# Optimization experiments

Measured on AMD Instinct MI355X. Metric: run time of the kernel, lower is better.

## Reference

```python
import jax, jax.numpy as jnp
import numpy as np

REG_MAX = 16
NC = 80
TOPK = 10
ALPHA = 1.0
BETA = 6.0
BOX_W, CLS_W, DFL_W = 7.5, 0.5, 1.5
IMG = 1280.0


def _ciou(b1, b2, eps=1e-7):
    # b1, b2: [..., 4] xyxy, broadcastable
    b1x1, b1y1, b1x2, b1y2 = b1[..., 0], b1[..., 1], b1[..., 2], b1[..., 3]
    b2x1, b2y1, b2x2, b2y2 = b2[..., 0], b2[..., 1], b2[..., 2], b2[..., 3]
    w1, h1 = b1x2 - b1x1, b1y2 - b1y1
    w2, h2 = b2x2 - b2x1, b2y2 - b2y1
    inter = (jnp.maximum(jnp.minimum(b1x2, b2x2) - jnp.maximum(b1x1, b2x1), 0.0) *
             jnp.maximum(jnp.minimum(b1y2, b2y2) - jnp.maximum(b1y1, b2y1), 0.0))
    union = w1 * h1 + w2 * h2 - inter + eps
    iou = inter / union
    cw = jnp.maximum(b1x2, b2x2) - jnp.minimum(b1x1, b2x1)
    ch = jnp.maximum(b1y2, b2y2) - jnp.minimum(b1y1, b2y1)
    c2 = cw * cw + ch * ch + eps
    rho2 = ((b2x1 + b2x2 - b1x1 - b1x2) ** 2 + (b2y1 + b2y2 - b1y1 - b1y2) ** 2) / 4.0
    v = (4.0 / np.pi ** 2) * (jnp.arctan(w2 / (h2 + eps)) - jnp.arctan(w1 / (h1 + eps))) ** 2
    alpha = jax.lax.stop_gradient(v / (v - iou + (1.0 + eps)))
    return iou - (rho2 / c2 + v * alpha)


def _loss(p0, p1, p2, gt_boxes, gt_labels, strides):
    preds = [p0, p1, p2]
    B = p0.shape[0]
    aps, sts, pds, pcs = [], [], [], []
    for i, p in enumerate(preds):
        H, W = p.shape[2], p.shape[3]
        gy, gx = jnp.meshgrid(jnp.arange(H, dtype=p.dtype) + 0.5,
                              jnp.arange(W, dtype=p.dtype) + 0.5, indexing='ij')
        aps.append(jnp.stack([gx.ravel(), gy.ravel()], -1))          # [HW,2] feat units
        sts.append(jnp.ones((H * W, 1), p.dtype) * strides[i])       # [HW,1]
        pds.append(p[:, :4 * REG_MAX].reshape(B, 4, REG_MAX, H * W).transpose(0, 3, 1, 2))
        pcs.append(p[:, 4 * REG_MAX:].transpose(0, 2, 3, 1).reshape(B, H * W, NC))
    ap = jnp.concatenate(aps)                 # [N,2]
    st = jnp.concatenate(sts)                 # [N,1]
    pred_dist = jnp.concatenate(pds, axis=1)  # [B,N,4,R]
    pred_cls = jnp.concatenate(pcs, axis=1)   # [B,N,NC]
    proj = jnp.arange(REG_MAX, dtype=p0.dtype)
    M = gt_boxes.shape[1]
    N = ap.shape[0]

    def one_image(pd, pc, gb, gl):
        # decode boxes (image units)
        dist = jnp.einsum('nkr,r->nk', jax.nn.softmax(pd, -1), proj)        # [N,4]
        pred_boxes = jnp.concatenate([(ap - dist[:, :2]) * st,
                                      (ap + dist[:, 2:]) * st], -1)          # [N,4]
        # ---- TaskAlignedAssigner (no grad) ----
        sg = jax.lax.stop_gradient
        pb, ps, gbs = sg(pred_boxes), sg(jax.nn.sigmoid(pc)), sg(gb)
        ap_img = ap * st                                                     # [N,2]
        in_gt = ((ap_img[:, None, 0] >= gbs[None, :, 0]) & (ap_img[:, None, 0] <= gbs[None, :, 2]) &
                 (ap_img[:, None, 1] >= gbs[None, :, 1]) & (ap_img[:, None, 1] <= gbs[None, :, 3]))
        ious = jnp.maximum(_ciou(pb[:, None, :], gbs[None, :, :]), 0.0)      # [N,M]
        align = (ps[:, gl] ** ALPHA) * (ious ** BETA) * in_gt
        align = align / (align.max(0, keepdims=True) + 1e-9)
        align = align * (ious > 0.1)
        # topk anchors per GT; anchor takes the GT with max masked score
        #  sequential loop with strict '>' updates)
        vals, idx = jax.lax.top_k(align.T, TOPK)                             # [M,TOPK]
        masked = jnp.zeros((M, N), align.dtype).at[
            jnp.arange(M)[:, None], idx].set(jnp.where(vals > 0, vals, 0.0))
        col = masked.T                                                       # [N,M]
        best_gt = jnp.argmax(col, 1)
        best_score = col.max(1)
        fg = (best_score > 0).astype(pd.dtype)                               # [N]
        num_fg = jnp.maximum(fg.sum(), 1.0)
        labels = gl[best_gt]
        boxes = gbs[best_gt]
        # ---- box (CIoU) loss over fg ----
        box_loss = ((1.0 - _ciou(pred_boxes, boxes)) * fg).sum() / num_fg
        # ---- DFL loss over fg ----
        t = jnp.concatenate([ap - boxes[:, :2] / st, boxes[:, 2:] / st - ap], -1)
        t = jnp.clip(t, 0.0, REG_MAX - 1 - 0.01)   # box2dist clamp
        t = jnp.clip(t, 0.0, REG_MAX - 1e-4)       # DFLLoss clamp
        left = jnp.floor(t).astype(jnp.int32)
        right = jnp.minimum(left + 1, REG_MAX - 1)
        wl = right.astype(t.dtype) - t
        wr = t - left.astype(t.dtype)
        logp = jax.nn.log_softmax(pd, -1)                                    # [N,4,R]
        ce_l = -jnp.take_along_axis(logp, left[..., None], -1)[..., 0]
        ce_r = -jnp.take_along_axis(logp, right[..., None], -1)[..., 0]
        dfl_loss = ((ce_l * wl + ce_r * wr) * fg[:, None]).sum() / (num_fg * 4.0)
        # ---- cls BCE-with-logits over all anchors ----
        cls_t = jax.nn.one_hot(labels, NC, dtype=pc.dtype) * (best_score * fg)[:, None]
        cls_loss = (jnp.logaddexp(0.0, pc) - pc * cls_t).sum(1).mean()
        has_fg = (fg.sum() > 0).astype(pd.dtype)
        return box_loss * has_fg, cls_loss * has_fg, dfl_loss * has_fg

    bl, cl, dl = jax.vmap(one_image)(pred_dist, pred_cls, gt_boxes, gt_labels)
    return BOX_W * bl.sum() + CLS_W * cl.sum() + DFL_W * dl.sum()


def setup_inputs() -> dict:
    key = jax.random.key(0)
    ks = jax.random.split(key, 6)
    p0 = jax.random.normal(ks[0], (8, 144, 160, 160), jnp.float32)
    p1 = jax.random.normal(ks[1], (8, 144, 80, 80), jnp.float32)
    p2 = jax.random.normal(ks[2], (8, 144, 40, 40), jnp.float32)
    cxcy = jax.random.uniform(ks[3], (8, 32, 2), minval=64.0, maxval=IMG - 64.0)
    wh = jax.random.uniform(ks[4], (8, 32, 2), minval=16.0, maxval=256.0)
    gt_boxes = jnp.clip(jnp.concatenate([cxcy - wh / 2, cxcy + wh / 2], -1), 0.0, IMG)
    gt_labels = jax.random.randint(ks[5], (8, 32), 0, NC)
    strides = jnp.array([8.0, 16.0, 32.0], jnp.float32)
    return {"p0": p0, "p1": p1, "p2": p2, "gt_boxes": gt_boxes,
            "gt_labels": gt_labels, "strides": strides}


def reference(p0, p1, p2, gt_boxes, gt_labels, strides):
    return _loss(p0, p1, p2, gt_boxes, gt_labels, strides)
```

## Files before the change

### kernel.cpp

```cpp
#include <hip/hip_runtime.h>
#include <cstdint>

#define NANCHOR 33600
#define BATCH   8
#define MGT     32
#define NCLS    80
#define MAXFG   (BATCH * MGT * 10)

struct AInfo {
    const float* ch0;
    int   hw;
    float apx, apy, st;
};

__device__ __forceinline__ AInfo anchor_info(const float* p0, const float* p1,
                                             const float* p2, int b, int n) {
    AInfo r;
    if (n < 25600) {
        int nn = n;
        r.ch0 = p0 + (size_t)b * (144 * 25600) + nn;
        r.hw = 25600; r.st = 8.f;
        r.apx = (float)(nn % 160) + 0.5f;
        r.apy = (float)(nn / 160) + 0.5f;
    } else if (n < 32000) {
        int nn = n - 25600;
        r.ch0 = p1 + (size_t)b * (144 * 6400) + nn;
        r.hw = 6400; r.st = 16.f;
        r.apx = (float)(nn % 80) + 0.5f;
        r.apy = (float)(nn / 80) + 0.5f;
    } else {
        int nn = n - 32000;
        r.ch0 = p2 + (size_t)b * (144 * 1600) + nn;
        r.hw = 1600; r.st = 32.f;
        r.apx = (float)(nn % 40) + 0.5f;
        r.apy = (float)(nn / 40) + 0.5f;
    }
    return r;
}

__device__ __forceinline__ float ciou_f(float b1x1, float b1y1, float b1x2, float b1y2,
                                        float g1x, float g1y, float g2x, float g2y) {
    const float eps = 1e-7f;
    float w1 = b1x2 - b1x1, h1 = b1y2 - b1y1;
    float w2 = g2x - g1x,   h2 = g2y - g1y;
    float iw = fminf(b1x2, g2x) - fmaxf(b1x1, g1x);
    float ih = fminf(b1y2, g2y) - fmaxf(b1y1, g1y);
    float inter = fmaxf(iw, 0.f) * fmaxf(ih, 0.f);
    float uni = w1 * h1 + w2 * h2 - inter + eps;
    float iou = inter / uni;
    float cw = fmaxf(b1x2, g2x) - fminf(b1x1, g1x);
    float ch = fmaxf(b1y2, g2y) - fminf(b1y1, g1y);
    float c2 = cw * cw + ch * ch + eps;
    float dx = g1x + g2x - b1x1 - b1x2;
    float dy = g1y + g2y - b1y1 - b1y2;
    float rho2 = (dx * dx + dy * dy) * 0.25f;
    float t = atanf(w2 / (h2 + eps)) - atanf(w1 / (h1 + eps));
    float v = 0.40528473456935108577f * t * t;
    float alpha = v / (v - iou + (1.f + eps));
    return iou - (rho2 / c2 + v * alpha);
}

__device__ __forceinline__ float fast_splus(float x) {
    return fmaxf(x, 0.f) + __logf(1.f + __expf(-fabsf(x)));
}
__device__ __forceinline__ float sp4(float4 x) {
    return fast_splus(x.x) + fast_splus(x.y) + fast_splus(x.z) + fast_splus(x.w);
}


__global__ void k_init(float* acc) {
    acc[threadIdx.x] = 0.f;
}

__global__ __launch_bounds__(128) void k_decode(const float* __restrict__ p0,
                                                const float* __restrict__ p1,
                                                const float* __restrict__ p2,
                                                float2* __restrict__ pb2,
                                                unsigned long long* __restrict__ best,
                                                float* __restrict__ acc) {
    int b = blockIdx.y;
    int role = blockIdx.z;
    int t = blockIdx.x * 128 + threadIdx.x;

    if (role >= 2) {
        float s0 = 0.f, s1 = 0.f, s2 = 0.f, s3 = 0.f;
        if (t < NANCHOR / 4) {
            int n = t * 4;
            const float* ch0; int hw;
            if (n < 25600)      { ch0 = p0 + (size_t)b * (144 * 25600) + n;          hw = 25600; }
            else if (n < 32000) { ch0 = p1 + (size_t)b * (144 * 6400) + (n - 25600); hw = 6400; }
            else                { ch0 = p2 + (size_t)b * (144 * 1600) + (n - 32000); hw = 1600; }
            const float* cp = ch0 + (size_t)(64 + (role - 2) * 20) * hw;
#pragma unroll
            for (int c = 0; c < 20; c += 4) {
                float4 x0 = *(const float4*)(cp + (size_t)(c + 0) * hw);
                float4 x1 = *(const float4*)(cp + (size_t)(c + 1) * hw);
                float4 x2 = *(const float4*)(cp + (size_t)(c + 2) * hw);
                float4 x3 = *(const float4*)(cp + (size_t)(c + 3) * hw);
                s0 += sp4(x0); s1 += sp4(x1); s2 += sp4(x2); s3 += sp4(x3);
            }
        }
        float sp = (s0 + s1) + (s2 + s3);
#pragma unroll
        for (int o = 32; o > 0; o >>= 1) sp += __shfl_down(sp, o, 64);
        if ((threadIdx.x & 63) == 0) atomicAdd(&acc[b * 8 + 0], sp);
        return;
    }

    if (t >= NANCHOR / 4) return;
    int n = t * 4;
    const float* ch0; int hw; float st, apx, apy;
    if (n < 25600) {
        ch0 = p0 + (size_t)b * (144 * 25600) + n;
        hw = 25600; st = 8.f;
        apx = (float)(n % 160) + 0.5f; apy = (float)(n / 160) + 0.5f;
    } else if (n < 32000) {
        int nn = n - 25600;
        ch0 = p1 + (size_t)b * (144 * 6400) + nn;
        hw = 6400; st = 16.f;
        apx = (float)(nn % 80) + 0.5f; apy = (float)(nn / 80) + 0.5f;
    } else {
        int nn = n - 32000;
        ch0 = p2 + (size_t)b * (144 * 1600) + nn;
        hw = 1600; st = 32.f;
        apx = (float)(nn % 40) + 0.5f; apy = (float)(nn / 40) + 0.5f;
    }

    int k0 = role * 2;
    const float* cA = ch0 + (size_t)(k0 * 16) * hw;
    const float* cB = cA + (size_t)16 * hw;
    float4 sA = make_float4(0.f, 0.f, 0.f, 0.f), wA = sA, sB = sA, wB = sA;
#pragma unroll
    for (int r = 0; r < 16; r++) {
        float4 a = *(const float4*)(cA + (size_t)r * hw);
        float4 c = *(const float4*)(cB + (size_t)r * hw);
        float fr = (float)r;
        float eax = __expf(a.x), eay = __expf(a.y), eaz = __expf(a.z), eaw = __expf(a.w);
        float ecx = __expf(c.x), ecy = __expf(c.y), ecz = __expf(c.z), ecw = __expf(c.w);
        sA.x += eax; sA.y += eay; sA.z += eaz; sA.w += eaw;
        sB.x += ecx; sB.y += ecy; sB.z += ecz; sB.w += ecw;
        wA.x = fmaf(eax, fr, wA.x); wA.y = fmaf(eay, fr, wA.y);
        wA.z = fmaf(eaz, fr, wA.z); wA.w = fmaf(eaw, fr, wA.w);
        wB.x = fmaf(ecx, fr, wB.x); wB.y = fmaf(ecy, fr, wB.y);
        wB.z = fmaf(ecz, fr, wB.z); wB.w = fmaf(ecw, fr, wB.w);
    }
    float dA[4] = { wA.x / sA.x, wA.y / sA.y, wA.z / sA.z, wA.w / sA.w };
    float dB[4] = { wB.x / sB.x, wB.y / sB.y, wB.z / sB.z, wB.w / sB.w };

    size_t base = (size_t)b * NANCHOR + n;
    if (role == 0) {
#pragma unroll
        for (int i = 0; i < 4; i++) {
            float ax = apx + (float)i;
            pb2[(base + i) * 2 + 0] = make_float2((ax - dA[i]) * st, (apy - dB[i]) * st);
        }
#pragma unroll
        for (int i = 0; i < 4; i++) best[base + i] = 0ull;
    } else {
#pragma unroll
        for (int i = 0; i < 4; i++) {
            float ax = apx + (float)i;
            pb2[(base + i) * 2 + 1] = make_float2((ax + dA[i]) * st, (apy + dB[i]) * st);
        }
    }
}

__global__ __launch_bounds__(256) void k_assign(const float* __restrict__ p0,
                                                const float* __restrict__ p1,
                                                const float* __restrict__ p2,
                                                const float4* __restrict__ pb,
                                                const float* __restrict__ gtb,
                                                const int* __restrict__ gtl,
                                                unsigned long long* __restrict__ best,
                                                float* __restrict__ acc,
                                                uint2* __restrict__ fglist) {
    int bm = blockIdx.x;
    int b = bm >> 5, m = bm & 31;
    const float* g = gtb + (size_t)(b * MGT + m) * 4;
    float g0 = g[0], g1 = g[1], g2 = g[2], g3 = g[3];
    int label = gtl[b * MGT + m];
    int tid = threadIdx.x;

    float tv[10];
    int   ti[10];
#pragma unroll
    for (int j = 0; j < 10; j++) { tv[j] = -1.f; ti[j] = 0x7fffffff; }
    float maxu = 0.f;

    const int   LW[3]   = {160, 80, 40};
    const int   LOFF[3] = {0, 25600, 32000};
    const float LST[3]  = {8.f, 16.f, 32.f};

    for (int l = 0; l < 3; l++) {
        float st = LST[l];
        int W = LW[l];
        float inv_st = 1.f / st;
        int ix0 = max(0,     (int)floorf(g0 * inv_st - 0.5f) - 1);
        int ix1 = min(W - 1, (int)ceilf (g2 * inv_st - 0.5f) + 1);
        int iy0 = max(0,     (int)floorf(g1 * inv_st - 0.5f) - 1);
        int iy1 = min(W - 1, (int)ceilf (g3 * inv_st - 0.5f) + 1);
        int nx = ix1 - ix0 + 1, ny = iy1 - iy0 + 1;
        if (nx <= 0 || ny <= 0) continue;
        int cnt = nx * ny;
        const float* lp = (l == 0) ? p0 : (l == 1) ? p1 : p2;
        int hw = W * W;
        const float* ch0 = lp + (size_t)b * 144 * hw;
        const float* pcls = ch0 + (size_t)(64 + label) * hw;

        for (int idx = tid; idx < cnt; idx += 256) {
            int iy = iy0 + idx / nx;
            int ix = ix0 + idx % nx;
            float ax = ((float)ix + 0.5f) * st;
            float ay = ((float)iy + 0.5f) * st;
            if (ax < g0 || ax > g2 || ay < g1 || ay > g3) continue;
            int nn = iy * W + ix;
            int n = LOFF[l] + nn;
            float4 box = pb[(size_t)b * NANCHOR + n];
            float c = ciou_f(box.x, box.y, box.z, box.w, g0, g1, g2, g3);
            float iou = fmaxf(c, 0.f);
            if (iou <= 0.f) continue;
            float pcv = pcls[nn];
            float ps = 1.f / (1.f + __expf(-pcv));
            float i2 = iou * iou;
            float a = ps * i2 * i2 * i2;
            maxu = fmaxf(maxu, a);
            if (iou > 0.1f && a > tv[9]) {
                tv[9] = a; ti[9] = n;
#pragma unroll
                for (int j = 9; j > 0; --j) {
                    if (tv[j] > tv[j - 1]) {
                        float tf = tv[j]; tv[j] = tv[j - 1]; tv[j - 1] = tf;
                        int   tt = ti[j]; ti[j] = ti[j - 1]; ti[j - 1] = tt;
                    }
                }
            }
        }
    }

    __shared__ float sval[2560];
    __shared__ int   sidx[2560];
    __shared__ float rv[256];
    __shared__ int   ra[256];
    __shared__ int   rs[256];
    __shared__ float smax[256];
    __shared__ int   winners[10];
    __shared__ int   nwin;

#pragma unroll
    for (int j = 0; j < 10; j++) {
        sval[tid * 10 + j] = tv[j];
        sidx[tid * 10 + j] = ti[j];
    }
    smax[tid] = maxu;
    if (tid == 0) nwin = 0;
    __syncthreads();
    for (int s = 128; s > 0; s >>= 1) {
        if (tid < s) smax[tid] = fmaxf(smax[tid], smax[tid + s]);
        __syncthreads();
    }
    float denom = smax[0] + 1e-9f;

    for (int r = 0; r < 10; r++) {
        float bv = -1.f; int ba = 0x7fffffff; int bs = -1;
#pragma unroll
        for (int j = 0; j < 10; j++) {
            int s0 = tid * 10 + j;
            float v = sval[s0]; int a0 = sidx[s0];
            if (v > bv || (v == bv && a0 < ba)) { bv = v; ba = a0; bs = s0; }
        }
        rv[tid] = bv; ra[tid] = ba; rs[tid] = bs;
        __syncthreads();
        for (int s = 128; s > 0; s >>= 1) {
            if (tid < s) {
                if (rv[tid + s] > rv[tid] ||
                    (rv[tid + s] == rv[tid] && ra[tid + s] < ra[tid])) {
                    rv[tid] = rv[tid + s]; ra[tid] = ra[tid + s]; rs[tid] = rs[tid + s];
                }
            }
            __syncthreads();
        }
        if (tid == 0 && rv[0] > 0.f) {
            float nv = rv[0] / denom;
            unsigned long long pk =
                ((unsigned long long)__float_as_uint(nv) << 32) |
                (unsigned long long)(31 - m);
            atomicMax(&best[(size_t)b * NANCHOR + ra[0]], pk);
            winners[nwin++] = ra[0];
            sval[rs[0]] = -1.f;
        }
        __syncthreads();
    }

    if (tid == 0 && nwin > 0) {
        unsigned int* list_cnt = (unsigned int*)(acc + 120);
        unsigned int base = atomicAdd(list_cnt, (unsigned int)nwin);
        for (int j = 0; j < nwin; j++)
            fglist[base + j] = make_uint2((unsigned int)(b * NANCHOR + winners[j]),
                                          (unsigned int)m);
    }
}

__global__ __launch_bounds__(256) void k_final(const float* __restrict__ p0,
                                               const float* __restrict__ p1,
                                               const float* __restrict__ p2,
                                               const float4* __restrict__ pb,
                                               const float* __restrict__ gtb,
                                               const int* __restrict__ gtl,
                                               const unsigned long long* __restrict__ best,
                                               const uint2* __restrict__ fglist,
                                               float* __restrict__ acc) {
    __shared__ float sacc[BATCH][4];
    int tid = threadIdx.x;
    if (tid < BATCH * 4) sacc[tid >> 2][tid & 3] = 0.f;
    __syncthreads();

    unsigned int cnt = *(const unsigned int*)(acc + 120);
    unsigned int j = blockIdx.x * 256 + tid;
    unsigned int i = j >> 2;
    int k = (int)(j & 3);
    if (i < cnt) {
        uint2 e = fglist[i];
        int bn = (int)e.x, m = (int)e.y;
        unsigned long long pk = best[bn];
        if ((unsigned int)(pk & 0xffffffffull) == (unsigned int)(31 - m)) {
            int b = bn / NANCHOR, n = bn % NANCHOR;
            const float* g = gtb + (size_t)(b * MGT + m) * 4;
            float g0 = g[0], g1 = g[1], g2 = g[2], g3 = g[3];
            AInfo ai = anchor_info(p0, p1, p2, b, n);
            float inv_st = 1.f / ai.st;
            float tk = (k == 0) ? ai.apx - g0 * inv_st
                     : (k == 1) ? ai.apy - g1 * inv_st
                     : (k == 2) ? g2 * inv_st - ai.apx
                     :            g3 * inv_st - ai.apy;
            float t = fminf(fmaxf(tk, 0.f), 14.99f);
            int left = (int)floorf(t);
            int right = (left + 1 < 15) ? left + 1 : 15;
            float wl = (float)right - t;
            float wr = t - (float)left;
            float v[16];
            float mx = -1e30f;
#pragma unroll
            for (int r = 0; r < 16; r++) {
                v[r] = ai.ch0[(size_t)(k * 16 + r) * ai.hw];
                mx = fmaxf(mx, v[r]);
            }
            float s = 0.f;
#pragma unroll
            for (int r = 0; r < 16; r++) s += __expf(v[r] - mx);
            float lse = mx + __logf(s);
            float dfl = (lse - v[left]) * wl + (lse - v[right]) * wr;
            atomicAdd(&sacc[b][1], dfl);

            if (k == 0) {
                float score = __uint_as_float((unsigned int)(pk >> 32));
                int label = gtl[b * MGT + m];
                float4 box = pb[bn];
                float c = ciou_f(box.x, box.y, box.z, box.w, g0, g1, g2, g3);
                float pcv = ai.ch0[(size_t)(64 + label) * ai.hw];
                atomicAdd(&sacc[b][0], 1.f - c);
                atomicAdd(&sacc[b][2], pcv * score);
                atomicAdd(&sacc[b][3], 1.f);
            }
        }
    }
    __syncthreads();
    if (tid < BATCH * 4) {
        float v = sacc[tid >> 2][tid & 3];
        if (v != 0.f) atomicAdd(&acc[(tid >> 2) * 8 + 1 + (tid & 3)], v);
    }
}

__global__ void k_combine(const float* __restrict__ acc, float* __restrict__ out) {
    if (blockIdx.x == 0 && threadIdx.x == 0) {
        float total = 0.f;
        for (int b = 0; b < BATCH; b++) {
            float nfr = acc[b * 8 + 4];
            float has = nfr > 0.f ? 1.f : 0.f;
            float nf = fmaxf(nfr, 1.f);
            float box_l = acc[b * 8 + 1] / nf;
            float cls_l = (acc[b * 8 + 0] - acc[b * 8 + 3]) / (float)NANCHOR;
            float dfl_l = acc[b * 8 + 2] / (nf * 4.f);
            total += has * (7.5f * box_l + 0.5f * cls_l + 1.5f * dfl_l);
        }
        out[0] = total;
    }
}

extern "C" void kernel_launch(void* const* d_in, const int* in_sizes, int n_in,
                              void* d_out, int out_size, void* d_ws, size_t ws_size,
                              hipStream_t stream) {
    (void)in_sizes; (void)n_in; (void)out_size; (void)ws_size;
    const float* p0  = (const float*)d_in[0];
    const float* p1  = (const float*)d_in[1];
    const float* p2  = (const float*)d_in[2];
    const float* gtb = (const float*)d_in[3];
    const int*   gtl = (const int*)d_in[4];

    char* ws = (char*)d_ws;
    unsigned long long* best = (unsigned long long*)ws;
    float4* pb = (float4*)(ws + (size_t)BATCH * NANCHOR * 8);
    float*  acc = (float*)(ws + (size_t)BATCH * NANCHOR * 8
                              + (size_t)BATCH * NANCHOR * 16);
    uint2* fglist = (uint2*)((char*)acc + 512);

    k_init   <<<1, 128, 0, stream>>>(acc);
    k_decode <<<dim3(66, BATCH, 6), 128, 0, stream>>>(p0, p1, p2, (float2*)pb, best, acc);
    k_assign <<<BATCH * MGT, 256, 0, stream>>>(p0, p1, p2, pb, gtb, gtl, best, acc, fglist);
    k_final  <<<(MAXFG * 4 + 255) / 256, 256, 0, stream>>>(p0, p1, p2, pb, gtb, gtl, best,
                                                           fglist, acc);
    k_combine<<<1, 64, 0, stream>>>(acc, (float*)d_out);
}
```

Before: 254.3 us.

## Fuse decode and softplus roles into one thread per anchor kernel

The old decode kernel split work across six block roles, each thread handling four anchors with float4 loads: two roles decoded box sides and four roles summed softplus over class channels. Now each thread handles one anchor and reads all 144 channels with scalar coalesced loads. It computes all four DFL expectations, the full softplus sum, writes one float4 box and clears the best slot. This drops the redundant per-role address setup and the split float2 writes, and gives more threads with less work each. The risks are scalar loads in place of float4, and a long serial chain of 144 loads per thread that may limit memory-level parallelism.

```diff
diff --git a/kernel.cpp b/kernel.cpp
--- a/kernel.cpp
+++ b/kernel.cpp
@@ -63,106 +63,76 @@
 __device__ __forceinline__ float fast_splus(float x) {
     return fmaxf(x, 0.f) + __logf(1.f + __expf(-fabsf(x)));
 }
-__device__ __forceinline__ float sp4(float4 x) {
-    return fast_splus(x.x) + fast_splus(x.y) + fast_splus(x.z) + fast_splus(x.w);
-}
 
 
 __global__ void k_init(float* acc) {
     acc[threadIdx.x] = 0.f;
 }
 
-__global__ __launch_bounds__(128) void k_decode(const float* __restrict__ p0,
-                                                const float* __restrict__ p1,
-                                                const float* __restrict__ p2,
-                                                float2* __restrict__ pb2,
-                                                unsigned long long* __restrict__ best,
-                                                float* __restrict__ acc) {
+__global__ __launch_bounds__(128, 4) void k_decode(const float* __restrict__ p0,
+                                                   const float* __restrict__ p1,
+                                                   const float* __restrict__ p2,
+                                                   float4* __restrict__ pb,
+                                                   unsigned long long* __restrict__ best,
+                                                   float* __restrict__ acc) {
     int b = blockIdx.y;
-    int role = blockIdx.z;
     int t = blockIdx.x * 128 + threadIdx.x;
-
-    if (role >= 2) {
+    float sp = 0.f;
+
+    if (t < NANCHOR) {
+        int n = t;
+        const float* q; int hw, W; float st; int nn;
+        if (n < 25600) {
+            nn = n;           q = p0 + (size_t)b * (144 * 25600) + nn;
+            hw = 25600; W = 160; st = 8.f;
+        } else if (n < 32000) {
+            nn = n - 25600;   q = p1 + (size_t)b * (144 * 6400) + nn;
+            hw = 6400;  W = 80;  st = 16.f;
+        } else {
+            nn = n - 32000;   q = p2 + (size_t)b * (144 * 1600) + nn;
+            hw = 1600;  W = 40;  st = 32.f;
+        }
+
         float s0 = 0.f, s1 = 0.f, s2 = 0.f, s3 = 0.f;
-        if (t < NANCHOR / 4) {
-            int n = t * 4;
-            const float* ch0; int hw;
-            if (n < 25600)      { ch0 = p0 + (size_t)b * (144 * 25600) + n;          hw = 25600; }
-            else if (n < 32000) { ch0 = p1 + (size_t)b * (144 * 6400) + (n - 25600); hw = 6400; }
-            else                { ch0 = p2 + (size_t)b * (144 * 1600) + (n - 32000); hw = 1600; }
-            const float* cp = ch0 + (size_t)(64 + (role - 2) * 20) * hw;
-#pragma unroll
-            for (int c = 0; c < 20; c += 4) {
-                float4 x0 = *(const float4*)(cp + (size_t)(c + 0) * hw);
-                float4 x1 = *(const float4*)(cp + (size_t)(c + 1) * hw);
-                float4 x2 = *(const float4*)(cp + (size_t)(c + 2) * hw);
-                float4 x3 = *(const float4*)(cp + (size_t)(c + 3) * hw);
-                s0 += sp4(x0); s1 += sp4(x1); s2 += sp4(x2); s3 += sp4(x3);
-            }
-        }
-        float sp = (s0 + s1) + (s2 + s3);
-#pragma unroll
-        for (int o = 32; o > 0; o >>= 1) sp += __shfl_down(sp, o, 64);
-        if ((threadIdx.x & 63) == 0) atomicAdd(&acc[b * 8 + 0], sp);
-        return;
-    }
-
-    if (t >= NANCHOR / 4) return;
-    int n = t * 4;
-    const float* ch0; int hw; float st, apx, apy;
-    if (n < 25600) {
-        ch0 = p0 + (size_t)b * (144 * 25600) + n;
-        hw = 25600; st = 8.f;
-        apx = (float)(n % 160) + 0.5f; apy = (float)(n / 160) + 0.5f;
-    } else if (n < 32000) {
-        int nn = n - 25600;
-        ch0 = p1 + (size_t)b * (144 * 6400) + nn;
-        hw = 6400; st = 16.f;
-        apx = (float)(nn % 80) + 0.5f; apy = (float)(nn / 80) + 0.5f;
-    } else {
-        int nn = n - 32000;
-        ch0 = p2 + (size_t)b * (144 * 1600) + nn;
-        hw = 1600; st = 32.f;
-        apx = (float)(nn % 40) + 0.5f; apy = (float)(nn / 40) + 0.5f;
-    }
-
-    int k0 = role * 2;
-    const float* cA = ch0 + (size_t)(k0 * 16) * hw;
-    const float* cB = cA + (size_t)16 * hw;
-    float4 sA = make_float4(0.f, 0.f, 0.f, 0.f), wA = sA, sB = sA, wB = sA;
-#pragma unroll
-    for (int r = 0; r < 16; r++) {
-        float4 a = *(const float4*)(cA + (size_t)r * hw);
-        float4 c = *(const float4*)(cB + (size_t)r * hw);
-        float fr = (float)r;
-        float eax = __expf(a.x), eay = __expf(a.y), eaz = __expf(a.z), eaw = __expf(a.w);
-        float ecx = __expf(c.x), ecy = __expf(c.y), ecz = __expf(c.z), ecw = __expf(c.w);
-        sA.x += eax; sA.y += eay; sA.z += eaz; sA.w += eaw;
-        sB.x += ecx; sB.y += ecy; sB.z += ecz; sB.w += ecw;
-        wA.x = fmaf(eax, fr, wA.x); wA.y = fmaf(eay, fr, wA.y);
-        wA.z = fmaf(eaz, fr, wA.z); wA.w = fmaf(eaw, fr, wA.w);
-        wB.x = fmaf(ecx, fr, wB.x); wB.y = fmaf(ecy, fr, wB.y);
-        wB.z = fmaf(ecz, fr, wB.z); wB.w = fmaf(ecw, fr, wB.w);
-    }
-    float dA[4] = { wA.x / sA.x, wA.y / sA.y, wA.z / sA.z, wA.w / sA.w };
-    float dB[4] = { wB.x / sB.x, wB.y / sB.y, wB.z / sB.z, wB.w / sB.w };
-
-    size_t base = (size_t)b * NANCHOR + n;
-    if (role == 0) {
-#pragma unroll
-        for (int i = 0; i < 4; i++) {
-            float ax = apx + (float)i;
-            pb2[(base + i) * 2 + 0] = make_float2((ax - dA[i]) * st, (apy - dB[i]) * st);
-        }
-#pragma unroll
-        for (int i = 0; i < 4; i++) best[base + i] = 0ull;
-    } else {
-#pragma unroll
-        for (int i = 0; i < 4; i++) {
-            float ax = apx + (float)i;
-            pb2[(base + i) * 2 + 1] = make_float2((ax + dA[i]) * st, (apy + dB[i]) * st);
-        }
-    }
+        float w0 = 0.f, w1 = 0.f, w2 = 0.f, w3 = 0.f;
+#pragma unroll
+        for (int r = 0; r < 16; r++) {
+            float v0 = q[(size_t)(r)      * hw];
+            float v1 = q[(size_t)(16 + r) * hw];
+            float v2 = q[(size_t)(32 + r) * hw];
+            float v3 = q[(size_t)(48 + r) * hw];
+            float fr = (float)r;
+            float e0 = __expf(v0), e1 = __expf(v1), e2 = __expf(v2), e3 = __expf(v3);
+            s0 += e0; s1 += e1; s2 += e2; s3 += e3;
+            w0 = fmaf(e0, fr, w0); w1 = fmaf(e1, fr, w1);
+            w2 = fmaf(e2, fr, w2); w3 = fmaf(e3, fr, w3);
+        }
+        float d0 = w0 / s0, d1 = w1 / s1, d2 = w2 / s2, d3 = w3 / s3;
+
+        const float* qc = q + (size_t)64 * hw;
+        float a0 = 0.f, a1 = 0.f, a2 = 0.f, a3 = 0.f;
+#pragma unroll
+        for (int c = 0; c < 80; c += 4) {
+            float x0 = qc[(size_t)(c + 0) * hw];
+            float x1 = qc[(size_t)(c + 1) * hw];
+            float x2 = qc[(size_t)(c + 2) * hw];
+            float x3 = qc[(size_t)(c + 3) * hw];
+            a0 += fast_splus(x0); a1 += fast_splus(x1);
+            a2 += fast_splus(x2); a3 += fast_splus(x3);
+        }
+        sp = (a0 + a1) + (a2 + a3);
+
+        float apx = (float)(nn % W) + 0.5f;
+        float apy = (float)(nn / W) + 0.5f;
+        size_t bn = (size_t)b * NANCHOR + n;
+        pb[bn] = make_float4((apx - d0) * st, (apy - d1) * st,
+                             (apx + d2) * st, (apy + d3) * st);
+        best[bn] = 0ull;
+    }
+
+#pragma unroll
+    for (int o = 32; o > 0; o >>= 1) sp += __shfl_down(sp, o, 64);
+    if ((threadIdx.x & 63) == 0) atomicAdd(&acc[b * 8 + 0], sp);
 }
 
 __global__ __launch_bounds__(256) void k_assign(const float* __restrict__ p0,
@@ -404,7 +374,7 @@
     uint2* fglist = (uint2*)((char*)acc + 512);
 
     k_init   <<<1, 128, 0, stream>>>(acc);
-    k_decode <<<dim3(66, BATCH, 6), 128, 0, stream>>>(p0, p1, p2, (float2*)pb, best, acc);
+    k_decode <<<dim3((NANCHOR + 127) / 128, BATCH), 128, 0, stream>>>(p0, p1, p2, pb, best, acc);
     k_assign <<<BATCH * MGT, 256, 0, stream>>>(p0, p1, p2, pb, gtb, gtl, best, acc, fglist);
     k_final  <<<(MAXFG * 4 + 255) / 256, 256, 0, stream>>>(p0, p1, p2, pb, gtb, gtl, best,
                                                            fglist, acc);
```

After: 318.0 us. +25.0%, slower.
